# Kernel optimization log

Hardware: AMD Instinct MI355X
Metric: run time of the kernel (lower is better)

The kernel has to match this reference:

```python
import jax, jax.numpy as jnp
import numpy as np

LSTM = 256
NUM_CELLS = 5
BLOCKS = 6
TEMP = 5.0
TANH_C = 1.1


def setup_inputs() -> dict:
    key = jax.random.key(0)
    ks = jax.random.split(key, 8)
    s = 0.05  # small init so sigmoids/tanh stay in sane range
    return {
        "enc_w": jax.random.normal(ks[0], (5, LSTM), jnp.float32) * s,
        "w_ih": jax.random.normal(ks[1], (4 * LSTM, LSTM), jnp.float32) * s,
        "w_hh": jax.random.normal(ks[2], (4 * LSTM, LSTM), jnp.float32) * s,
        "b_ih": jax.random.normal(ks[3], (4 * LSTM,), jnp.float32) * s,
        "b_hh": jax.random.normal(ks[4], (4 * LSTM,), jnp.float32) * s,
        "w1": jax.random.normal(ks[5], (LSTM, LSTM), jnp.float32) * s,
        "w2": jax.random.normal(ks[6], (LSTM, LSTM), jnp.float32) * s,
        "v": jax.random.normal(ks[7], (LSTM,), jnp.float32) * s,
    }


def _lstm_cell(x, h, c, w_ih, w_hh, b_ih, b_hh):
    # torch.nn.LSTMCell gate order: i, f, g, o
    g = w_ih @ x + b_ih + w_hh @ h + b_hh  # [4*LSTM]
    i, f, gg, o = jnp.split(g, 4)
    i, f, o = jax.nn.sigmoid(i), jax.nn.sigmoid(f), jax.nn.sigmoid(o)
    c2 = f * c + i * jnp.tanh(gg)
    h2 = o * jnp.tanh(c2)
    return h2, c2


def _run_sampler(bkey, enc_w, w_ih, w_hh, b_ih, b_hh, w1, w2, v):
    zeros = jnp.zeros((LSTM,), jnp.float32)
    inputs = enc_w[0]  # encoder(0)
    anchors = []
    anchors_w1 = []
    prev_h = prev_c = zeros
    # first two layers: LSTM always fed zero state (faithful to source)
    for _ in range(2):
        prev_h, prev_c = _lstm_cell(inputs, zeros, zeros, w_ih, w_hh, b_ih, b_hh)
        anchors.append(zeros)
        anchors_w1.append(w1 @ prev_h)
    arc_seq, log_probs, entropies = [], [], []
    step = 0
    for layer_id in range(2, NUM_CELLS + 2):
        for _ in range(2):
            prev_h, prev_c = _lstm_cell(inputs, prev_h, prev_c, w_ih, w_hh, b_ih, b_hh)
            q = jnp.tanh(jnp.stack(anchors_w1[:layer_id]) + w2 @ prev_h)  # [layer_id, LSTM]
            logits = (q @ v) / TEMP  # [layer_id]
            logits = TANH_C * jnp.tanh(logits)
            skey = jax.random.fold_in(bkey, step); step += 1
            index = jax.random.categorical(skey, logits)
            lsm = jax.nn.log_softmax(logits)
            arc_seq.append(index)
            log_probs.append(-lsm[index])  # F.cross_entropy
            entropies.append(jax.lax.stop_gradient(-jnp.sum(lsm * jnp.exp(lsm))))
            inputs = jnp.stack(anchors[:layer_id])[index]
        prev_h, prev_c = _lstm_cell(inputs, prev_h, prev_c, w_ih, w_hh, b_ih, b_hh)
        anchors.append(prev_h)
        anchors_w1.append(w1 @ prev_h)
        inputs = enc_w[0]
    arc = jnp.stack(arc_seq)  # [2*NUM_CELLS] int
    return arc, sum(entropies), sum(log_probs), prev_c, prev_h


def reference(enc_w, w_ih, w_hh, b_ih, b_hh, w1, w2, v):
    key = jax.random.key(42)
    all_arc = []
    all_entropy = jnp.float32(0.0)
    all_log_prob = jnp.float32(0.0)
    c = h = None
    for b in range(BLOCKS):
        arc, ent, lp, c, h = _run_sampler(
            jax.random.fold_in(key, b), enc_w, w_ih, w_hh, b_ih, b_hh, w1, w2, v)
        all_arc.append(arc)
        all_entropy = all_entropy + ent
        all_log_prob = all_log_prob + lp
    return (jnp.stack(all_arc), all_log_prob, all_entropy, c[None, :], h[None, :])
```

## Files before the change

kernel.cpp:

```cpp
#include <hip/hip_runtime.h>
#include <stdint.h>


#define NBLK  6
#define PWG   8
#define THR   512
#define TINYF 1.17549435e-38f
#define HTAGB 0xC3B00000u
#define YTAGB 0xE1700000u
#define ITAGB 0xA5D00000u
#define DONE_MAGIC 0x444f4e45

typedef unsigned long long u64;
struct U2 { uint32_t x, y; };

#define W_DONE 0u
#define W_PART 64u
#define W_IDX  128u
#define W_HX   640u
#define W_YMB  25216u
#define W_NEED 126976u

#define S_READY 0u
#define S_DONE  192u
#define S_PART  224u
#define S_HP    320u
#define S_ACC   24896u
#define FXS     67108864.0f
#define READY_MAGIC 0x52454459

__device__ __forceinline__ U2 tf2x32(uint32_t k0, uint32_t k1,
                                     uint32_t c0, uint32_t c1) {
  uint32_t ks2 = k0 ^ k1 ^ 0x1BD11BDAu;
  uint32_t x0 = c0 + k0, x1 = c1 + k1;
#define TFR(r) { x0 += x1; x1 = (x1 << (r)) | (x1 >> (32 - (r))); x1 ^= x0; }
  TFR(13) TFR(15) TFR(26) TFR(6)   x0 += k1;  x1 += ks2 + 1u;
  TFR(17) TFR(29) TFR(16) TFR(24)  x0 += ks2; x1 += k0 + 2u;
  TFR(13) TFR(15) TFR(26) TFR(6)   x0 += k0;  x1 += k1 + 3u;
  TFR(17) TFR(29) TFR(16) TFR(24)  x0 += k1;  x1 += ks2 + 4u;
  TFR(13) TFR(15) TFR(26) TFR(6)   x0 += ks2; x1 += k0 + 5u;
#undef TFR
  U2 r; r.x = x0; r.y = x1; return r;
}

__device__ __forceinline__ float sigf(float x) {
  return 1.0f / (1.0f + expf(-x));
}
__device__ __forceinline__ void istore(int* p, int v) {
  __hip_atomic_store(p, v, __ATOMIC_RELAXED, __HIP_MEMORY_SCOPE_AGENT);
}
__device__ __forceinline__ int iload(const int* p) {
  return __hip_atomic_load(p, __ATOMIC_RELAXED, __HIP_MEMORY_SCOPE_AGENT);
}
__device__ __forceinline__ void hstore(u64* p, u64 v) {
  __hip_atomic_store(p, v, __ATOMIC_RELAXED, __HIP_MEMORY_SCOPE_AGENT);
}
__device__ __forceinline__ u64 hload(const u64* p) {
  return __hip_atomic_load(p, __ATOMIC_RELAXED, __HIP_MEMORY_SCOPE_AGENT);
}
__device__ __forceinline__ void fstore(float* p, float v) {
  __hip_atomic_store(p, v, __ATOMIC_RELAXED, __HIP_MEMORY_SCOPE_AGENT);
}
__device__ __forceinline__ float fload(const float* p) {
  return __hip_atomic_load(p, __ATOMIC_RELAXED, __HIP_MEMORY_SCOPE_AGENT);
}
__device__ __forceinline__ u64 pollw(const u64* p, uint32_t want) {
  u64 v;
  for (;;) {
    v = hload(p);
    if ((uint32_t)(v >> 32) == want) return v;
    __builtin_amdgcn_s_sleep(1);
  }
}

__global__ __launch_bounds__(THR, 2) void ctrl_v11(
    const float* __restrict__ enc_w,
    const float* __restrict__ wih,
    const float* __restrict__ whh,
    const float* __restrict__ b_ih,
    const float* __restrict__ b_hh,
    const float* __restrict__ w1,
    const float* __restrict__ w2,
    const float* __restrict__ vvec,
    unsigned char* __restrict__ ws,
    float* __restrict__ out) {

  const int b = blockIdx.x & 7;
  const int p = blockIdx.x >> 3;
  if (b >= NBLK) return;
  const int tid = threadIdx.x;

  int*   done = (int*)(ws + W_DONE);
  float* part = (float*)(ws + W_PART);
  u64*   idxw = (u64*)(ws + W_IDX);
  u64*   hx   = (u64*)(ws + W_HX);
  u64*   ymb  = (u64*)(ws + W_YMB);

  const int rl = tid & 127, s = tid >> 7;
  const int grow = (rl >> 5) * 256 + p * 32 + (rl & 31);
  const int k0 = s * 64;
  const int rr = tid & 255, ks = tid >> 8;
  const int cb = p * 32 + ks * 16;

  __shared__ __align__(16) float gateL[THR];
  __shared__ __align__(16) float hL[256], encL[256], vL[256];
  __shared__ __align__(16) float anchL[4][256];
  __shared__ __align__(16) float w2hS[256], aw1S[6][256];
  __shared__ __align__(16) float yL8[8][256];
  __shared__ float rowSumL[128], biasS[128], h2S[32];
  __shared__ float logitL[8];
  __shared__ int   selL;

  if (tid < 256) { encL[tid] = enc_w[tid]; vL[tid] = vvec[tid]; }
  if (tid < 128) {
    int r = (tid >> 5) * 256 + p * 32 + (tid & 31);
    biasS[tid] = b_ih[r] + b_hh[r];
  }

  float4 wihr[16], whhr[16];
  #pragma unroll
  for (int c = 0; c < 16; ++c) {
    wihr[c] = *(const float4*)(wih + grow * 256 + k0 + c * 4);
    whhr[c] = *(const float4*)(whh + grow * 256 + k0 + c * 4);
  }
  float w1c[16], w2c[16];
  #pragma unroll
  for (int j = 0; j < 16; ++j) {
    w1c[j] = w1[rr * 256 + cb + j];
    w2c[j] = w2[rr * 256 + cb + j];
  }
  __syncthreads();

  auto dotIH = [&](const float* x) {
    float a = 0.0f;
    #pragma unroll
    for (int c = 0; c < 16; ++c) {
      float4 xv = *(const float4*)(x + k0 + c * 4);
      float4 w = wihr[c];
      a += w.x * xv.x + w.y * xv.y + w.z * xv.z + w.w * xv.w;
    }
    return a;
  };
  auto dotHH = [&]() {
    float a = 0.0f;
    #pragma unroll
    for (int c = 0; c < 16; ++c) {
      float4 xv = *(const float4*)(hL + k0 + c * 4);
      float4 w = whhr[c];
      a += w.x * xv.x + w.y * xv.y + w.z * xv.z + w.w * xv.w;
    }
    return a;
  };

  const float encih = dotIH(encL);

  float cv = 0.0f;
  U2 bk = tf2x32(0u, 42u, 0u, (uint32_t)b);
  int k = 1, step = 0;
  float lpAcc = 0.0f, entAcc = 0.0f;

  auto cell = [&](float gacc, int mode, int aid, int cid) {
    gateL[tid] = gacc;
    __syncthreads();
    if (tid < 128) {
      float ssum = 0.0f;
      #pragma unroll
      for (int j = 0; j < 4; ++j) ssum += gateL[j * 128 + tid];
      rowSumL[tid] = ssum + biasS[tid];
    }
    __syncthreads();
    if (tid < 32) {
      float gi = rowSumL[tid],       gf = rowSumL[32 + tid];
      float gg2 = rowSumL[64 + tid], go = rowSumL[96 + tid];
      float c2 = sigf(gf) * cv + sigf(gi) * tanhf(gg2);
      float h2 = sigf(go) * tanhf(c2);
      cv = c2;
      h2S[tid] = h2;
      if (mode == 2) {
        if (b == NBLK - 1) { out[62 + p * 32 + tid] = cv; out[318 + p * 32 + tid] = h2; }
      } else {
        hstore(&hx[(k & 1) * 1536 + b * 256 + p * 32 + tid],
               ((u64)(HTAGB | (uint32_t)k) << 32) | (u64)__float_as_uint(h2));
      }
    }
    __syncthreads();
    if (mode == 2) return;

    {
      const float* wc = (mode == 1) ? w1c : w2c;
      float yp = 0.0f;
      #pragma unroll
      for (int j = 0; j < 16; ++j) yp += wc[j] * h2S[ks * 16 + j];
      gateL[tid] = yp;
    }
    __syncthreads();
    u64* mslot = ymb + (size_t)(k & 1) * 6192 + (b * 8 + p) * 129;
    if (tid < 128) {
      float ya = gateL[2 * tid]     + gateL[256 + 2 * tid];
      float yb = gateL[2 * tid + 1] + gateL[256 + 2 * tid + 1];
      hstore(mslot + tid,
             ((u64)__float_as_uint(yb) << 32) | (u64)__float_as_uint(ya));
    }
    __syncthreads();
    if (tid == 0)
      hstore(mslot + 128, ((u64)(YTAGB | (uint32_t)k) << 32) | 1u);

    if (tid < 256) {
      u64 v = pollw(&hx[(k & 1) * 1536 + b * 256 + tid], HTAGB | (uint32_t)k);
      float hv = __uint_as_float((uint32_t)v);
      hL[tid] = hv;
      if (mode == 1 && cid >= 0) anchL[cid][tid] = hv;
    }
    __syncthreads();

    if (p == 0) {
      if (tid < 8)
        pollw(ymb + (size_t)(k & 1) * 6192 + (b * 8 + tid) * 129 + 128,
              YTAGB | (uint32_t)k);
      __syncthreads();
      {
        int pw = tid >> 6, o = tid & 63;
        const u64* mb = ymb + (size_t)(k & 1) * 6192 + (b * 8 + pw) * 129;
        u64 wa = hload(mb + 2 * o), wb = hload(mb + 2 * o + 1);
        yL8[pw][4 * o + 0] = __uint_as_float((uint32_t)wa);
        yL8[pw][4 * o + 1] = __uint_as_float((uint32_t)(wa >> 32));
        yL8[pw][4 * o + 2] = __uint_as_float((uint32_t)wb);
        yL8[pw][4 * o + 3] = __uint_as_float((uint32_t)(wb >> 32));
      }
      __syncthreads();
      if (tid < 256) {
        float y = 0.0f;
        #pragma unroll
        for (int pw = 0; pw < 8; ++pw) y += yL8[pw][tid];
        if (mode == 1) aw1S[aid][tid] = y; else w2hS[tid] = y;
      }
      __syncthreads();
    }
    ++k;
  };

  auto resolve = [&](int L) -> int {
    if (p == 0) {
      int wv = tid >> 6, lane = tid & 63;
      if (wv < L) {
        float a = 0.0f;
        #pragma unroll
        for (int j = 0; j < 4; ++j) {
          int kk = j * 64 + lane;
          a += tanhf(aw1S[wv][kk] + w2hS[kk]) * vL[kk];
        }
        a += __shfl_down(a, 32);
        a += __shfl_down(a, 16);
        a += __shfl_down(a, 8);
        a += __shfl_down(a, 4);
        a += __shfl_down(a, 2);
        a += __shfl_down(a, 1);
        if (lane == 0) logitL[wv] = a;
      }
      __syncthreads();
      if (tid < 64) {
        float lg = 0.0f, sgum = -1e30f;
        if (tid < L) {
          lg = 1.1f * tanhf(logitL[tid] * 0.2f);
          U2 sk = tf2x32(bk.x, bk.y, 0u, (uint32_t)step);
          U2 r2 = tf2x32(sk.x, sk.y, 0u, (uint32_t)tid);
          uint32_t bits = r2.x ^ r2.y;
          float u = __uint_as_float((bits >> 9) | 0x3f800000u) - 1.0f;
          u = fmaxf(TINYF, u + TINYF);
          sgum = lg - logf(-logf(u));
        }
        int bi = 0;
        float best = __shfl(sgum, 0, 64);
        for (int j = 1; j < L; ++j) {
          float sj = __shfl(sgum, j, 64);
          if (sj > best) { best = sj; bi = j; }
        }
        float mx = __shfl(lg, 0, 64);
        for (int j = 1; j < L; ++j) mx = fmaxf(mx, __shfl(lg, j, 64));
        float se = 0.0f;
        for (int j = 0; j < L; ++j) se += expf(__shfl(lg, j, 64) - mx);
        float lse = logf(se);
        float lgbi = __shfl(lg, bi, 64);
        float es = 0.0f;
        for (int j = 0; j < L; ++j) {
          float l = __shfl(lg, j, 64) - mx - lse;
          es += l * expf(l);
        }
        if (tid == 0) {
          lpAcc += -(lgbi - mx - lse);
          entAcc += -es;
          selL = bi;
          out[b * 10 + step] = (float)bi;
          hstore(&idxw[b * 10 + step],
                 ((u64)(ITAGB | (uint32_t)step) << 32) | (u64)(uint32_t)bi);
        }
      }
      __syncthreads();
    } else {
      if (tid == 0) {
        u64 v = pollw(&idxw[b * 10 + step], ITAGB | (uint32_t)step);
        selL = (int)(uint32_t)v;
      }
      __syncthreads();
    }
    step++;
    return selL;
  };

  cell(encih, 1, 0, -1);
  if (p == 0) {
    if (tid < 256) aw1S[1][tid] = aw1S[0][tid];
    __syncthreads();
  }

  for (int L = 2; L <= 6; ++L) {
    { float hh = dotHH(); cell(encih + hh, 0, 0, -1); }
    {
      int s1; float hh;
      if (p == 0) { s1 = resolve(L); hh = dotHH(); }
      else        { hh = dotHH(); s1 = resolve(L); }
      float a = (s1 >= 2) ? dotIH(&anchL[s1 - 2][0]) : 0.0f;
      cell(a + hh, 0, 0, -1);
    }
    {
      int s2; float hh;
      if (p == 0) { s2 = resolve(L); hh = dotHH(); }
      else        { hh = dotHH(); s2 = resolve(L); }
      float a = (s2 >= 2) ? dotIH(&anchL[s2 - 2][0]) : 0.0f;
      if (L < 6) cell(a + hh, 1, L, L - 2);
      else       cell(a + hh, 2, 0, -1);
    }
  }

  if (p == 0 && tid == 0) {
    fstore(&part[2 * b], lpAcc);
    fstore(&part[2 * b + 1], entAcc);
    __builtin_amdgcn_s_waitcnt(0);
    istore(&done[b], DONE_MAGIC);
    if (b == NBLK - 1) {
      float lp = 0.0f, en = 0.0f;
      for (int j = 0; j < NBLK; ++j) {
        while (iload(&done[j]) != DONE_MAGIC) __builtin_amdgcn_s_sleep(1);
        lp += fload(&part[2 * j]);
        en += fload(&part[2 * j + 1]);
      }
      out[60] = lp;
      out[61] = en;
    }
  }
}

__global__ __launch_bounds__(1024) void ctrl_small(
    const float* __restrict__ enc_w,
    const float* __restrict__ wih,
    const float* __restrict__ whh,
    const float* __restrict__ b_ih,
    const float* __restrict__ b_hh,
    const float* __restrict__ w1,
    const float* __restrict__ w2,
    const float* __restrict__ vvec,
    unsigned char* __restrict__ ws,
    float* __restrict__ out) {

  const int b = blockIdx.x & 7;
  const int p = blockIdx.x >> 3;
  if (b >= NBLK) return;
  const int tid = threadIdx.x;

  int*   ready = (int*)(ws + S_READY);
  int*   done  = (int*)(ws + S_DONE);
  float* part  = (float*)(ws + S_PART);
  u64*   hp    = (u64*)(ws + S_HP);
  int*   acc   = (int*)(ws + S_ACC);

  const int rl = tid >> 3, s = tid & 7;
  const int g = rl >> 5, el = rl & 31;
  const int row = g * 256 + p * 32 + el;
  const int k0 = s * 32;
  const int rr = tid & 255, ks = tid >> 8;

  __shared__ __align__(16) float hL[256], encL[256], vL[256];
  __shared__ __align__(16) float anchL[4][256];
  __shared__ __align__(16) float partL[1024];
  __shared__ __align__(16) float w2hS[256], aw1S[6][256];
  __shared__ float rowSumL[128], biasS[128], h2S[32];
  __shared__ float logitL[8];
  __shared__ int   selL;

  if (tid < 256) { encL[tid] = enc_w[tid]; vL[tid] = vvec[tid]; }
  if (tid < 128) {
    int gg = tid >> 5, ee = tid & 31, r = gg * 256 + p * 32 + ee;
    biasS[tid] = b_ih[r] + b_hh[r];
  }

  float4 wihr[8], whhr[8];
  #pragma unroll
  for (int c = 0; c < 8; ++c) {
    int cc = (c + s) & 7;
    wihr[c] = *(const float4*)(wih + row * 256 + k0 + cc * 4);
    whhr[c] = *(const float4*)(whh + row * 256 + k0 + cc * 4);
  }
  float w1c[8], w2c[8];
  #pragma unroll
  for (int j = 0; j < 8; ++j) {
    w1c[j] = w1[rr * 256 + p * 32 + ks * 8 + j];
    w2c[j] = w2[rr * 256 + p * 32 + ks * 8 + j];
  }

  if (tid < 32) istore(&acc[1 * (NBLK * 256) + b * 256 + p * 32 + tid], 0);
  __syncthreads();
  if (tid == 0) istore(&ready[b * 8 + p], READY_MAGIC);
  if (tid < 8) {
    while (iload(&ready[b * 8 + tid]) != READY_MAGIC)
      __builtin_amdgcn_s_sleep(1);
  }
  __syncthreads();

  auto dotIH = [&](const float* x) {
    float a = 0.0f;
    #pragma unroll
    for (int c = 0; c < 8; ++c) {
      int cc = (c + s) & 7;
      float4 xv = *(const float4*)(x + k0 + cc * 4);
      float4 w = wihr[c];
      a += w.x * xv.x + w.y * xv.y + w.z * xv.z + w.w * xv.w;
    }
    return a;
  };
  auto dotHH = [&]() {
    float a = 0.0f;
    #pragma unroll
    for (int c = 0; c < 8; ++c) {
      int cc = (c + s) & 7;
      float4 xv = *(const float4*)(hL + k0 + cc * 4);
      float4 w = whhr[c];
      a += w.x * xv.x + w.y * xv.y + w.z * xv.z + w.w * xv.w;
    }
    return a;
  };

  const float encih = dotIH(encL);
  float cv = 0.0f;
  U2 bk = tf2x32(0u, 42u, 0u, (uint32_t)b);
  int k = 1, step = 0;
  float lpAcc = 0.0f, entAcc = 0.0f;

  auto cell = [&](float gacc, int mode, int aid, int cid) {
    partL[tid] = gacc;
    __syncthreads();
    if (tid < 128) {
      float ssum = 0.0f;
      #pragma unroll
      for (int j = 0; j < 8; ++j) ssum += partL[tid * 8 + j];
      rowSumL[tid] = ssum + biasS[tid];
    }
    __syncthreads();
    if (tid < 32) {
      float gi = rowSumL[tid],       gf = rowSumL[32 + tid];
      float gg2 = rowSumL[64 + tid], go = rowSumL[96 + tid];
      float c2 = sigf(gf) * cv + sigf(gi) * tanhf(gg2);
      float h2 = sigf(go) * tanhf(c2);
      cv = c2;
      h2S[tid] = h2;
      if (mode == 2 && b == NBLK - 1) {
        out[62 + p * 32 + tid] = cv;
        out[318 + p * 32 + tid] = h2;
      }
    }
    __syncthreads();
    if (mode == 2) return;
    {
      const float* wc = (mode == 1) ? w1c : w2c;
      float yp = 0.0f;
      #pragma unroll
      for (int j = 0; j < 8; ++j) yp += wc[j] * h2S[ks * 8 + j];
      atomicAdd(&acc[(k % 3) * (NBLK * 256) + b * 256 + rr],
                __float2int_rn(yp * FXS));
      if (tid < 32)
        istore(&acc[((k + 1) % 3) * (NBLK * 256) + b * 256 + p * 32 + tid], 0);
    }
    __syncthreads();
    if (tid < 32) {
      u64 pk = ((u64)(uint32_t)k << 32) | (u64)__float_as_uint(h2S[tid]);
      hstore(&hp[(k & 1) * (NBLK * 256) + b * 256 + p * 32 + tid], pk);
    }
    if (tid < 256) {
      u64 v;
      const u64* src = &hp[(k & 1) * (NBLK * 256) + b * 256 + tid];
      while ((int)(hload(src) >> 32) != k) __builtin_amdgcn_s_sleep(1);
      v = hload(src);
      float hv = __uint_as_float((uint32_t)v);
      hL[tid] = hv;
      if (mode == 1 && cid >= 0) anchL[cid][tid] = hv;
    }
    __syncthreads();
    if (tid < 256) {
      int iv = iload(&acc[(k % 3) * (NBLK * 256) + b * 256 + tid]);
      float f = (float)((double)iv * (1.0 / 67108864.0));
      if (mode == 1) aw1S[aid][tid] = f; else w2hS[tid] = f;
    }
    __syncthreads();
    ++k;
  };

  auto sample = [&](int L) -> int {
    int wv = tid >> 6, lane = tid & 63;
    if (wv < L) {
      float a = 0.0f;
      #pragma unroll
      for (int j = 0; j < 4; ++j) {
        int kk = lane * 4 + j;
        a += tanhf(aw1S[wv][kk] + w2hS[kk]) * vL[kk];
      }
      a += __shfl_down(a, 32);
      a += __shfl_down(a, 16);
      a += __shfl_down(a, 8);
      a += __shfl_down(a, 4);
      a += __shfl_down(a, 2);
      a += __shfl_down(a, 1);
      if (lane == 0) logitL[wv] = a;
    }
    __syncthreads();
    if (tid < 64) {
      float lg = 0.0f, sgum = -1e30f;
      if (tid < L) {
        lg = 1.1f * tanhf(logitL[tid] * 0.2f);
        U2 sk = tf2x32(bk.x, bk.y, 0u, (uint32_t)step);
        U2 r2 = tf2x32(sk.x, sk.y, 0u, (uint32_t)tid);
        uint32_t bits = r2.x ^ r2.y;
        float u = __uint_as_float((bits >> 9) | 0x3f800000u) - 1.0f;
        u = fmaxf(TINYF, u + TINYF);
        sgum = lg - logf(-logf(u));
      }
      int bi = 0;
      float best = __shfl(sgum, 0, 64);
      for (int j = 1; j < L; ++j) {
        float sj = __shfl(sgum, j, 64);
        if (sj > best) { best = sj; bi = j; }
      }
      float mx = __shfl(lg, 0, 64);
      for (int j = 1; j < L; ++j) mx = fmaxf(mx, __shfl(lg, j, 64));
      float se = 0.0f;
      for (int j = 0; j < L; ++j) se += expf(__shfl(lg, j, 64) - mx);
      float lse = logf(se);
      float lgbi = __shfl(lg, bi, 64);
      float es = 0.0f;
      for (int j = 0; j < L; ++j) {
        float l = __shfl(lg, j, 64) - mx - lse;
        es += l * expf(l);
      }
      if (tid == 0) {
        lpAcc += -(lgbi - mx - lse);
        entAcc += -es;
        selL = bi;
        if (p == 0) out[b * 10 + step] = (float)bi;
      }
    }
    __syncthreads();
    step++;
    return selL;
  };

  cell(encih, 1, 0, -1);
  if (tid < 256) aw1S[1][tid] = aw1S[0][tid];
  __syncthreads();
  for (int L = 2; L <= 6; ++L) {
    cell(encih + dotHH(), 0, 0, -1);
    int s1v = sample(L);
    {
      float a = (s1v >= 2) ? dotIH(&anchL[s1v - 2][0]) : 0.0f;
      cell(a + dotHH(), 0, 0, -1);
    }
    int s2v = sample(L);
    {
      float a = (s2v >= 2) ? dotIH(&anchL[s2v - 2][0]) : 0.0f;
      if (L < 6) cell(a + dotHH(), 1, L, L - 2);
      else       cell(a + dotHH(), 2, 0, -1);
    }
  }
  if (p == 0 && tid == 0) {
    fstore(&part[2 * b], lpAcc);
    fstore(&part[2 * b + 1], entAcc);
    __builtin_amdgcn_s_waitcnt(0);
    istore(&done[b], DONE_MAGIC);
    if (b == NBLK - 1) {
      float lp = 0.0f, en = 0.0f;
      for (int j = 0; j < NBLK; ++j) {
        while (iload(&done[j]) != DONE_MAGIC) __builtin_amdgcn_s_sleep(1);
        lp += fload(&part[2 * j]);
        en += fload(&part[2 * j + 1]);
      }
      out[60] = lp;
      out[61] = en;
    }
  }
}

extern "C" void kernel_launch(void* const* d_in, const int* in_sizes, int n_in,
                              void* d_out, int out_size, void* d_ws, size_t ws_size,
                              hipStream_t stream) {
  const float* enc = (const float*)d_in[0];
  const float* wih = (const float*)d_in[1];
  const float* whh = (const float*)d_in[2];
  const float* bih = (const float*)d_in[3];
  const float* bhh = (const float*)d_in[4];
  const float* w1  = (const float*)d_in[5];
  const float* w2  = (const float*)d_in[6];
  const float* v   = (const float*)d_in[7];
  unsigned char* ws = (unsigned char*)d_ws;
  float* out = (float*)d_out;

  if (ws_size >= W_NEED) {
    ctrl_v11<<<dim3(64), dim3(THR), 0, stream>>>(
        enc, wih, whh, bih, bhh, w1, w2, v, ws, out);
  } else {
    ctrl_small<<<dim3(64), dim3(1024), 0, stream>>>(
        enc, wih, whh, bih, bhh, w1, w2, v, ws, out);
  }
}
```

Baseline: 153.0 us.

## Replicate attention/sampling in every workgroup to drop index broadcast round-trip

Every workgroup now gathers the partial W1/W2 projections from all eight peers itself and runs the attention, Gumbel sampling and log-softmax redundantly, instead of workgroup 0 computing the index and publishing it through global memory for the others to poll. The gate-row reduction switches to a 4-lane shuffle with a new thread-to-row mapping, and y partials are stored as tagged per-element words, so readers poll data directly without a separate ready flag. This removes one cross-workgroup handshake per sampling step and several barriers. In exchange it adds eightfold redundant attention compute, more global polling traffic, and a larger workspace requirement, which could send more inputs to the fallback path.

```diff
diff --git a/kernel.cpp b/kernel.cpp
--- a/kernel.cpp
+++ b/kernel.cpp
@@ -8,7 +8,6 @@
 #define TINYF 1.17549435e-38f
 #define HTAGB 0xC3B00000u
 #define YTAGB 0xE1700000u
-#define ITAGB 0xA5D00000u
 #define DONE_MAGIC 0x444f4e45
 
 typedef unsigned long long u64;
@@ -16,10 +15,9 @@
 
 #define W_DONE 0u
 #define W_PART 64u
-#define W_IDX  128u
-#define W_HX   640u
-#define W_YMB  25216u
-#define W_NEED 126976u
+#define W_HX   128u
+#define W_YMB  24704u
+#define W_NEED 221312u
 
 #define S_READY 0u
 #define S_DONE  192u
@@ -73,7 +71,7 @@
   }
 }
 
-__global__ __launch_bounds__(THR, 2) void ctrl_v11(
+__global__ __launch_bounds__(THR, 1) void ctrl_v12(
     const float* __restrict__ enc_w,
     const float* __restrict__ wih,
     const float* __restrict__ whh,
@@ -92,13 +90,12 @@
 
   int*   done = (int*)(ws + W_DONE);
   float* part = (float*)(ws + W_PART);
-  u64*   idxw = (u64*)(ws + W_IDX);
   u64*   hx   = (u64*)(ws + W_HX);
   u64*   ymb  = (u64*)(ws + W_YMB);
 
-  const int rl = tid & 127, s = tid >> 7;
-  const int grow = (rl >> 5) * 256 + p * 32 + (rl & 31);
-  const int k0 = s * 64;
+  const int r4 = tid >> 2, s4 = tid & 3;
+  const int grow = (r4 >> 5) * 256 + p * 32 + (r4 & 31);
+  const int k0 = s4 * 64;
   const int rr = tid & 255, ks = tid >> 8;
   const int cb = p * 32 + ks * 16;
 
@@ -106,7 +103,6 @@
   __shared__ __align__(16) float hL[256], encL[256], vL[256];
   __shared__ __align__(16) float anchL[4][256];
   __shared__ __align__(16) float w2hS[256], aw1S[6][256];
-  __shared__ __align__(16) float yL8[8][256];
   __shared__ float rowSumL[128], biasS[128], h2S[32];
   __shared__ float logitL[8];
   __shared__ int   selL;
@@ -160,14 +156,10 @@
   float lpAcc = 0.0f, entAcc = 0.0f;
 
   auto cell = [&](float gacc, int mode, int aid, int cid) {
-    gateL[tid] = gacc;
-    __syncthreads();
-    if (tid < 128) {
-      float ssum = 0.0f;
-      #pragma unroll
-      for (int j = 0; j < 4; ++j) ssum += gateL[j * 128 + tid];
-      rowSumL[tid] = ssum + biasS[tid];
-    }
+    float a1 = __shfl_xor(gacc, 1);
+    float a2 = __shfl_xor(gacc, 2);
+    float a3 = __shfl_xor(gacc, 3);
+    if (s4 == 0) rowSumL[r4] = ((gacc + a1) + a2) + a3 + biasS[r4];
     __syncthreads();
     if (tid < 32) {
       float gi = rowSumL[tid],       gf = rowSumL[32 + tid];
@@ -194,138 +186,114 @@
       gateL[tid] = yp;
     }
     __syncthreads();
-    u64* mslot = ymb + (size_t)(k & 1) * 6192 + (b * 8 + p) * 129;
-    if (tid < 128) {
-      float ya = gateL[2 * tid]     + gateL[256 + 2 * tid];
-      float yb = gateL[2 * tid + 1] + gateL[256 + 2 * tid + 1];
-      hstore(mslot + tid,
-             ((u64)__float_as_uint(yb) << 32) | (u64)__float_as_uint(ya));
-    }
-    __syncthreads();
-    if (tid == 0)
-      hstore(mslot + 128, ((u64)(YTAGB | (uint32_t)k) << 32) | 1u);
-
+
+    const uint32_t wantY = YTAGB | (uint32_t)k;
+    const uint32_t wantH = HTAGB | (uint32_t)k;
+    u64* yslot = ymb + (size_t)(k & 1) * 12288 + (size_t)b * 2048;
     if (tid < 256) {
-      u64 v = pollw(&hx[(k & 1) * 1536 + b * 256 + tid], HTAGB | (uint32_t)k);
+      float yp2 = gateL[tid] + gateL[256 + tid];
+      hstore(yslot + p * 256 + tid,
+             ((u64)wantY << 32) | (u64)__float_as_uint(yp2));
+      u64 v = pollw(&hx[(k & 1) * 1536 + b * 256 + tid], wantH);
       float hv = __uint_as_float((uint32_t)v);
       hL[tid] = hv;
       if (mode == 1 && cid >= 0) anchL[cid][tid] = hv;
-    }
-    __syncthreads();
-
-    if (p == 0) {
-      if (tid < 8)
-        pollw(ymb + (size_t)(k & 1) * 6192 + (b * 8 + tid) * 129 + 128,
-              YTAGB | (uint32_t)k);
-      __syncthreads();
-      {
-        int pw = tid >> 6, o = tid & 63;
-        const u64* mb = ymb + (size_t)(k & 1) * 6192 + (b * 8 + pw) * 129;
-        u64 wa = hload(mb + 2 * o), wb = hload(mb + 2 * o + 1);
-        yL8[pw][4 * o + 0] = __uint_as_float((uint32_t)wa);
-        yL8[pw][4 * o + 1] = __uint_as_float((uint32_t)(wa >> 32));
-        yL8[pw][4 * o + 2] = __uint_as_float((uint32_t)wb);
-        yL8[pw][4 * o + 3] = __uint_as_float((uint32_t)(wb >> 32));
-      }
-      __syncthreads();
-      if (tid < 256) {
-        float y = 0.0f;
+    } else {
+      const int e = tid & 255;
+      const u64* bp = yslot + e;
+      u64 w[8];
+      for (;;) {
+        bool ok = true;
         #pragma unroll
-        for (int pw = 0; pw < 8; ++pw) y += yL8[pw][tid];
-        if (mode == 1) aw1S[aid][tid] = y; else w2hS[tid] = y;
-      }
-      __syncthreads();
-    }
+        for (int q = 0; q < 8; ++q) {
+          w[q] = hload(bp + q * 256);
+          ok &= ((uint32_t)(w[q] >> 32) == wantY);
+        }
+        if (ok) break;
+        __builtin_amdgcn_s_sleep(1);
+      }
+      float y = 0.0f;
+      #pragma unroll
+      for (int q = 0; q < 8; ++q) y += __uint_as_float((uint32_t)w[q]);
+      if (mode == 1) aw1S[aid][e] = y; else w2hS[e] = y;
+    }
+    __syncthreads();
     ++k;
   };
 
   auto resolve = [&](int L) -> int {
-    if (p == 0) {
-      int wv = tid >> 6, lane = tid & 63;
-      if (wv < L) {
-        float a = 0.0f;
-        #pragma unroll
-        for (int j = 0; j < 4; ++j) {
-          int kk = j * 64 + lane;
-          a += tanhf(aw1S[wv][kk] + w2hS[kk]) * vL[kk];
-        }
-        a += __shfl_down(a, 32);
-        a += __shfl_down(a, 16);
-        a += __shfl_down(a, 8);
-        a += __shfl_down(a, 4);
-        a += __shfl_down(a, 2);
-        a += __shfl_down(a, 1);
-        if (lane == 0) logitL[wv] = a;
-      }
-      __syncthreads();
-      if (tid < 64) {
-        float lg = 0.0f, sgum = -1e30f;
-        if (tid < L) {
-          lg = 1.1f * tanhf(logitL[tid] * 0.2f);
-          U2 sk = tf2x32(bk.x, bk.y, 0u, (uint32_t)step);
-          U2 r2 = tf2x32(sk.x, sk.y, 0u, (uint32_t)tid);
-          uint32_t bits = r2.x ^ r2.y;
-          float u = __uint_as_float((bits >> 9) | 0x3f800000u) - 1.0f;
-          u = fmaxf(TINYF, u + TINYF);
-          sgum = lg - logf(-logf(u));
-        }
-        int bi = 0;
-        float best = __shfl(sgum, 0, 64);
-        for (int j = 1; j < L; ++j) {
-          float sj = __shfl(sgum, j, 64);
-          if (sj > best) { best = sj; bi = j; }
-        }
-        float mx = __shfl(lg, 0, 64);
-        for (int j = 1; j < L; ++j) mx = fmaxf(mx, __shfl(lg, j, 64));
-        float se = 0.0f;
-        for (int j = 0; j < L; ++j) se += expf(__shfl(lg, j, 64) - mx);
-        float lse = logf(se);
-        float lgbi = __shfl(lg, bi, 64);
-        float es = 0.0f;
-        for (int j = 0; j < L; ++j) {
-          float l = __shfl(lg, j, 64) - mx - lse;
-          es += l * expf(l);
-        }
-        if (tid == 0) {
-          lpAcc += -(lgbi - mx - lse);
-          entAcc += -es;
-          selL = bi;
-          out[b * 10 + step] = (float)bi;
-          hstore(&idxw[b * 10 + step],
-                 ((u64)(ITAGB | (uint32_t)step) << 32) | (u64)(uint32_t)bi);
-        }
-      }
-      __syncthreads();
-    } else {
+    int wv = tid >> 6, lane = tid & 63;
+    if (wv < L) {
+      float a = 0.0f;
+      #pragma unroll
+      for (int j = 0; j < 4; ++j) {
+        int kk = j * 64 + lane;
+        a += tanhf(aw1S[wv][kk] + w2hS[kk]) * vL[kk];
+      }
+      a += __shfl_down(a, 32);
+      a += __shfl_down(a, 16);
+      a += __shfl_down(a, 8);
+      a += __shfl_down(a, 4);
+      a += __shfl_down(a, 2);
+      a += __shfl_down(a, 1);
+      if (lane == 0) logitL[wv] = a;
+    }
+    __syncthreads();
+    if (tid < 64) {
+      float lg = 0.0f, sgum = -1e30f;
+      if (tid < L) {
+        lg = 1.1f * tanhf(logitL[tid] * 0.2f);
+        U2 sk = tf2x32(bk.x, bk.y, 0u, (uint32_t)step);
+        U2 r2 = tf2x32(sk.x, sk.y, 0u, (uint32_t)tid);
+        uint32_t bits = r2.x ^ r2.y;
+        float u = __uint_as_float((bits >> 9) | 0x3f800000u) - 1.0f;
+        u = fmaxf(TINYF, u + TINYF);
+        sgum = lg - logf(-logf(u));
+      }
+      int bi = 0;
+      float best = __shfl(sgum, 0, 64);
+      for (int j = 1; j < L; ++j) {
+        float sj = __shfl(sgum, j, 64);
+        if (sj > best) { best = sj; bi = j; }
+      }
+      float mx = __shfl(lg, 0, 64);
+      for (int j = 1; j < L; ++j) mx = fmaxf(mx, __shfl(lg, j, 64));
+      float se = 0.0f;
+      for (int j = 0; j < L; ++j) se += expf(__shfl(lg, j, 64) - mx);
+      float lse = logf(se);
+      float lgbi = __shfl(lg, bi, 64);
+      float es = 0.0f;
+      for (int j = 0; j < L; ++j) {
+        float l = __shfl(lg, j, 64) - mx - lse;
+        es += l * expf(l);
+      }
       if (tid == 0) {
-        u64 v = pollw(&idxw[b * 10 + step], ITAGB | (uint32_t)step);
-        selL = (int)(uint32_t)v;
-      }
-      __syncthreads();
-    }
+        lpAcc += -(lgbi - mx - lse);
+        entAcc += -es;
+        selL = bi;
+        if (p == 0) out[b * 10 + step] = (float)bi;
+      }
+    }
+    __syncthreads();
     step++;
     return selL;
   };
 
   cell(encih, 1, 0, -1);
-  if (p == 0) {
-    if (tid < 256) aw1S[1][tid] = aw1S[0][tid];
-    __syncthreads();
-  }
+  if (tid < 256) aw1S[1][tid] = aw1S[0][tid];
+  __syncthreads();
 
   for (int L = 2; L <= 6; ++L) {
     { float hh = dotHH(); cell(encih + hh, 0, 0, -1); }
     {
-      int s1; float hh;
-      if (p == 0) { s1 = resolve(L); hh = dotHH(); }
-      else        { hh = dotHH(); s1 = resolve(L); }
+      float hh = dotHH();
+      int s1 = resolve(L);
       float a = (s1 >= 2) ? dotIH(&anchL[s1 - 2][0]) : 0.0f;
       cell(a + hh, 0, 0, -1);
     }
     {
-      int s2; float hh;
-      if (p == 0) { s2 = resolve(L); hh = dotHH(); }
-      else        { hh = dotHH(); s2 = resolve(L); }
+      float hh = dotHH();
+      int s2 = resolve(L);
       float a = (s2 >= 2) ? dotIH(&anchL[s2 - 2][0]) : 0.0f;
       if (L < 6) cell(a + hh, 1, L, L - 2);
       else       cell(a + hh, 2, 0, -1);
@@ -611,7 +579,7 @@
   float* out = (float*)d_out;
 
   if (ws_size >= W_NEED) {
-    ctrl_v11<<<dim3(64), dim3(THR), 0, stream>>>(
+    ctrl_v12<<<dim3(64), dim3(THR), 0, stream>>>(
         enc, wih, whh, bih, bhh, w1, w2, v, ws, out);
   } else {
     ctrl_small<<<dim3(64), dim3(1024), 0, stream>>>(
```

After: 175.1 us. +14.5%, slower.
